# Optimization experiments

Hardware: AMD Instinct MI355X
Metric: run time of the kernel (lower is better)

Reference implementation:

```python
import jax, jax.numpy as jnp
import numpy as np

VAR = (0.1, 0.2)          # encode variances (SSD convention used in MutualGuide)
F_ALPHA, F_GAMMA = 0.25, 1.0   # FocalLoss(alpha=0.25, gamma=1.0)
L_ALPHA, L_GAMMA, L_BETA = 0.5, 1.5, 0.11  # BalancedL1Loss

def point_form(p):
    # [P,4] cxcywh -> xyxy
    return jnp.concatenate([p[:, :2] - p[:, 2:] / 2, p[:, :2] + p[:, 2:] / 2], axis=1)

def jaccard(a, b):
    # a: [T,4] xyxy truths, b: [P,4] xyxy priors -> IoU [T,P]
    lt = jnp.maximum(a[:, None, :2], b[None, :, :2])
    rb = jnp.minimum(a[:, None, 2:], b[None, :, 2:])
    wh = jnp.clip(rb - lt, 0.0)
    inter = wh[..., 0] * wh[..., 1]
    area_a = ((a[:, 2] - a[:, 0]) * (a[:, 3] - a[:, 1]))[:, None]
    area_b = ((b[:, 2] - b[:, 0]) * (b[:, 3] - b[:, 1]))[None, :]
    return inter / (area_a + area_b - inter)

def match_one(truths, labels, priors_pt):
    # truths [T,4], labels [T] int, priors_pt [P,4]
    T = truths.shape[0]
    ov = jaccard(truths, priors_pt)                 # [T,P]
    best_truth_ov = ov.max(axis=0)                  # [P]
    best_truth_idx = ov.argmax(axis=0)              # [P]
    best_prior_idx = ov.argmax(axis=1)              # [T]
    # force each gt's best prior to be positive (index_fill_ with 2)
    best_truth_ov = best_truth_ov.at[best_prior_idx].set(2.0)
    best_truth_idx = best_truth_idx.at[best_prior_idx].set(jnp.arange(T))
    matches = truths[best_truth_idx]                # [P,4] xyxy
    conf = labels[best_truth_idx] + 1               # [P], 0 reserved for bg
    return matches, conf, best_truth_ov

def encode(matched, priors):
    # matched xyxy [N,4], priors cxcywh [N.,4]
    g_cxcy = ((matched[..., :2] + matched[..., 2:]) / 2 - priors[..., :2]) / (VAR[0] * priors[..., 2:])
    g_wh = jnp.log((matched[..., 2:] - matched[..., :2]) / priors[..., 2:]) / VAR[1]
    return jnp.concatenate([g_cxcy, g_wh], axis=-1)

def balanced_l1(pred, target):
    b = np.exp(L_GAMMA / L_ALPHA) - 1.0
    d = jnp.abs(pred - target)
    small = L_ALPHA / b * (b * d + 1.0) * jnp.log(b * d / L_BETA + 1.0) - L_ALPHA * d
    large = L_GAMMA * d + L_GAMMA / b - L_ALPHA * L_BETA
    return jnp.where(d < L_BETA, small, large)

def sigmoid_focal(logits, t):
    p = jax.nn.sigmoid(logits)
    ce = -(t * jax.nn.log_sigmoid(logits) + (1.0 - t) * jax.nn.log_sigmoid(-logits))
    pt = t * (1.0 - p) + (1.0 - t) * p
    w = (F_ALPHA * t + (1.0 - F_ALPHA) * (1.0 - t)) * pt ** F_GAMMA
    return w * ce

def setup_inputs() -> dict:
    key = jax.random.key(0)
    kl, kc, kp1, kp2, kt1, kt2, ktl = jax.random.split(key, 7)
    B, P, C, T = 16, 16384, 80, 32
    loc_data = jax.random.normal(kl, (B, P, 4), jnp.float32) * 0.1
    conf_data = jax.random.normal(kc, (B, P, C), jnp.float32)
    p_cxcy = jax.random.uniform(kp1, (P, 2), jnp.float32, 0.05, 0.95)
    p_wh = jax.random.uniform(kp2, (P, 2), jnp.float32, 0.02, 0.3)
    priors = jnp.concatenate([p_cxcy, p_wh], axis=1)
    t_c = jax.random.uniform(kt1, (B, T, 2), jnp.float32, 0.2, 0.8)
    t_wh = jax.random.uniform(kt2, (B, T, 2), jnp.float32, 0.05, 0.3)
    boxes = jnp.concatenate([jnp.clip(t_c - t_wh / 2, 0.0, 1.0), jnp.clip(t_c + t_wh / 2, 0.0, 1.0)], axis=-1)
    labels = jax.random.randint(ktl, (B, T), 0, C).astype(jnp.float32)
    targets = jnp.concatenate([boxes, labels[..., None]], axis=-1)  # [B,T,5]
    return {"loc_data": loc_data, "conf_data": conf_data, "priors": priors, "targets": targets}

def reference(loc_data, conf_data, priors, targets):
    B, P, C = conf_data.shape
    truths = targets[..., :4]
    labels = targets[..., 4].astype(jnp.int32)
    priors_pt = point_form(priors)
    loc_t, conf_t, overlap_t = jax.vmap(match_one, in_axes=(0, 0, None))(truths, labels, priors_pt)
    # masks (non-mutual-guide path)
    pos = overlap_t >= 0.5                                  # [B,P]
    ign = (overlap_t < 0.5) & (overlap_t >= 0.4)
    neg = overlap_t < 0.4
    # localization loss over positives (mean over masked elements)
    loc_targets = encode(loc_t, priors[None, :, :])          # [B,P,4]
    l1 = balanced_l1(loc_data, loc_targets)                  # [B,P,4]
    n_pos = jnp.maximum(pos.sum(), 1)
    loss_l = (l1 * pos[..., None]).sum() / (4.0 * n_pos)
    # classification: one-hot minus background, flip ignored rows to -1
    conf_t = jnp.where(neg, 0, conf_t)
    onehot = jax.nn.one_hot(conf_t, C + 1, dtype=conf_data.dtype)[..., 1:]  # [B,P,C]
    batch_label = jnp.where(ign[..., None], -onehot, onehot)
    mask = batch_label >= 0
    t = jnp.where(mask, batch_label, 0.0)
    fl = sigmoid_focal(conf_data, t)
    loss_c = (fl * mask).sum() / jnp.maximum(mask.sum(), 1)
    return (loss_l, loss_c)
```

## Files before the change

kernel.cpp:

```cpp
#include <hip/hip_runtime.h>

#pragma clang fp contract(off)

#define B_SZ 16
#define P_SZ 16384
#define C_SZ 80
#define T_SZ 32

struct Partial { float l; float c; unsigned pos; unsigned ign; };

__device__ __forceinline__ float iou_ref(float ax0, float ay0, float ax1, float ay1, float aarea,
                                         float bx0, float by0, float bx1, float by1, float barea) {
    float lx = fmaxf(ax0, bx0), ly = fmaxf(ay0, by0);
    float rx = fminf(ax1, bx1), ry = fminf(ay1, by1);
    float w = fmaxf(rx - lx, 0.0f), h = fmaxf(ry - ly, 0.0f);
    float inter = w * h;
    float denom = (aarea + barea) - inter;
    return inter / denom;
}

__global__ __launch_bounds__(256) void match_kernel(const float* __restrict__ priors,
                                                    const float* __restrict__ targets,
                                                    unsigned long long* __restrict__ keys) {
    const int b = blockIdx.y;
    const int p0 = blockIdx.x * 1024;
    const int tid = threadIdx.x;

    __shared__ float tx0[T_SZ], ty0[T_SZ], tx1[T_SZ], ty1[T_SZ], tar[T_SZ];
    __shared__ float red_ov[4][T_SZ];
    __shared__ int   red_ix[4][T_SZ];

    if (tid < T_SZ) {
        const float* tp = targets + (b * T_SZ + tid) * 5;
        float x0 = tp[0], y0 = tp[1], x1 = tp[2], y1 = tp[3];
        tx0[tid] = x0; ty0[tid] = y0; tx1[tid] = x1; ty1[tid] = y1;
        tar[tid] = (x1 - x0) * (y1 - y0);
    }
    __syncthreads();

    float bov[T_SZ];
    int   bpi[T_SZ];
#pragma unroll
    for (int t = 0; t < T_SZ; ++t) { bov[t] = -1.0f; bpi[t] = 0x7FFFFFFF; }

#pragma unroll
    for (int i = 0; i < 4; ++i) {
        int p = p0 + tid + i * 256;
        float4 pr = reinterpret_cast<const float4*>(priors)[p];
        float px0 = pr.x - pr.z * 0.5f, py0 = pr.y - pr.w * 0.5f;
        float px1 = pr.x + pr.z * 0.5f, py1 = pr.y + pr.w * 0.5f;
        float parea = (px1 - px0) * (py1 - py0);
#pragma unroll
        for (int t = 0; t < T_SZ; ++t) {
            float iou = iou_ref(tx0[t], ty0[t], tx1[t], ty1[t], tar[t], px0, py0, px1, py1, parea);
            if (iou > bov[t]) { bov[t] = iou; bpi[t] = p; }
        }
    }

    const int lane = tid & 63, wid = tid >> 6;
#pragma unroll
    for (int t = 0; t < T_SZ; ++t) {
        float v = bov[t]; int ix = bpi[t];
#pragma unroll
        for (int off = 32; off > 0; off >>= 1) {
            float v2 = __shfl_down(v, off, 64);
            int   i2 = __shfl_down(ix, off, 64);
            if (v2 > v || (v2 == v && i2 < ix)) { v = v2; ix = i2; }
        }
        if (lane == 0) { red_ov[wid][t] = v; red_ix[wid][t] = ix; }
    }
    __syncthreads();

    if (tid < T_SZ) {
        float v = red_ov[0][tid]; int ix = red_ix[0][tid];
#pragma unroll
        for (int w = 1; w < 4; ++w) {
            float v2 = red_ov[w][tid]; int i2 = red_ix[w][tid];
            if (v2 > v || (v2 == v && i2 < ix)) { v = v2; ix = i2; }
        }
        unsigned long long key = (((unsigned long long)__float_as_uint(v)) << 32)
                               | (unsigned long long)(0xFFFFFFFFu - (unsigned)ix);
        keys[(b * 16 + blockIdx.x) * T_SZ + tid] = key;
    }
}

__device__ __forceinline__ float bl1(float pred, float target) {
    const float bC   = (float)19.085536923187668;
    const float aob  = (float)(0.5 / 19.085536923187668);
    const float cL   = (float)(1.5 / 19.085536923187668 - 0.055);
    float d = fabsf(pred - target);
    if (d < 0.11f) {
        return aob * (bC * d + 1.0f) * __logf(bC * d / 0.11f + 1.0f) - 0.5f * d;
    }
    return 1.5f * d + cL;
}

__device__ __forceinline__ float focal(float x, bool isT) {
    float u  = __expf(-fabsf(x));
    float L  = __logf(1.0f + u);
    float q  = __builtin_amdgcn_rcpf(1.0f + u);
    float p  = (x >= 0.0f) ? q : 1.0f - q;
    float xp = fmaxf(x, 0.0f);
    float xn = xp - x;
    return isT ? 0.25f * (1.0f - p) * (xn + L) : 0.75f * p * (xp + L);
}

__global__ __launch_bounds__(256) void loss_kernel(const float* __restrict__ loc_data,
                                                   const float* __restrict__ conf_data,
                                                   const float* __restrict__ priors,
                                                   const float* __restrict__ targets,
                                                   const unsigned long long* __restrict__ keys,
                                                   Partial* __restrict__ partials) {
    const int b = blockIdx.y;
    const int p0 = blockIdx.x * 128;
    const int tid = threadIdx.x;

    __shared__ float tx0[T_SZ], ty0[T_SZ], tx1[T_SZ], ty1[T_SZ], tar[T_SZ];
    __shared__ int tlab[T_SZ], bp[T_SZ];
    __shared__ unsigned char flag_s[128];
    __shared__ unsigned char tcls_s[128];
    __shared__ unsigned char code_s[2560];
    __shared__ float rf_l[4], rf_c[4];
    __shared__ int ri_p[4], ri_i[4];

    if (tid < T_SZ) {
        const float* tp = targets + (b * T_SZ + tid) * 5;
        float x0 = tp[0], y0 = tp[1], x1 = tp[2], y1 = tp[3];
        tx0[tid] = x0; ty0[tid] = y0; tx1[tid] = x1; ty1[tid] = y1;
        tar[tid] = (x1 - x0) * (y1 - y0);
        tlab[tid] = (int)tp[4];
        const unsigned long long* kb = keys + b * 16 * T_SZ + tid;
        unsigned long long k = kb[0];
#pragma unroll
        for (int w = 1; w < 16; ++w) {
            unsigned long long k2 = kb[w * T_SZ];
            if (k2 > k) k = k2;
        }
        bp[tid] = (int)(0xFFFFFFFFu - (unsigned)(k & 0xFFFFFFFFull));
    }
    __syncthreads();

    float sum_l = 0.0f, sum_c = 0.0f;
    int pos_c = 0, ign_c = 0;

    if (tid < 128) {
        int p = p0 + tid;
        float4 pr = reinterpret_cast<const float4*>(priors)[p];
        float px0 = pr.x - pr.z * 0.5f, py0 = pr.y - pr.w * 0.5f;
        float px1 = pr.x + pr.z * 0.5f, py1 = pr.y + pr.w * 0.5f;
        float parea = (px1 - px0) * (py1 - py0);

        float ov = -1.0f; int idx = 0;
#pragma unroll
        for (int t = 0; t < T_SZ; ++t) {
            float iou = iou_ref(tx0[t], ty0[t], tx1[t], ty1[t], tar[t], px0, py0, px1, py1, parea);
            if (iou > ov) { ov = iou; idx = t; }
        }
#pragma unroll
        for (int t = 0; t < T_SZ; ++t) if (bp[t] == p) { ov = 2.0f; idx = t; }

        int fl = (ov >= 0.5f) ? 1 : ((ov >= 0.4f) ? 2 : 0);
        flag_s[tid] = (unsigned char)fl;
        tcls_s[tid] = (unsigned char)tlab[idx];

        if (fl == 1) {
            pos_c = 1;
            float4 ld = reinterpret_cast<const float4*>(loc_data)[b * P_SZ + p];
            float mx0 = tx0[idx], my0 = ty0[idx], mx1 = tx1[idx], my1 = ty1[idx];
            float gx = ((mx0 + mx1) * 0.5f - pr.x) / (0.1f * pr.z);
            float gy = ((my0 + my1) * 0.5f - pr.y) / (0.1f * pr.w);
            float gw = __logf((mx1 - mx0) / pr.z) / 0.2f;
            float gh = __logf((my1 - my0) / pr.w) / 0.2f;
            sum_l = bl1(ld.x, gx) + bl1(ld.y, gy) + bl1(ld.z, gw) + bl1(ld.w, gh);
        } else if (fl == 2) {
            ign_c = 1;
        }
    }
    __syncthreads();

#pragma unroll
    for (int jj = tid; jj < 2560; jj += 256) {
        int pl = jj / 20;
        int c0 = (jj - pl * 20) * 4;
        int f = flag_s[pl];
        int tc = tcls_s[pl];
        int g = tc - c0;
        int m = (g >= 0 && g < 4) ? (g + 1) : 0;
        code_s[jj] = (unsigned char)(f | (m << 2));
    }
    __syncthreads();

    const float4* cbase = reinterpret_cast<const float4*>(conf_data + ((size_t)(b * P_SZ + p0)) * C_SZ);
    float4 v[10];
#pragma unroll
    for (int it = 0; it < 10; ++it) v[it] = cbase[tid + it * 256];
    unsigned char cd[10];
#pragma unroll
    for (int it = 0; it < 10; ++it) cd[it] = code_s[tid + it * 256];

#pragma unroll
    for (int it = 0; it < 10; ++it) {
        int code = cd[it];
        int f = code & 3;
        int m = code >> 2;
        float s = 0.0f;
        {
            float fk = focal(v[it].x, (f == 1) && (m == 1));
            if (!((f == 2) && (m == 1))) s += fk;
        }
        {
            float fk = focal(v[it].y, (f == 1) && (m == 2));
            if (!((f == 2) && (m == 2))) s += fk;
        }
        {
            float fk = focal(v[it].z, (f == 1) && (m == 3));
            if (!((f == 2) && (m == 3))) s += fk;
        }
        {
            float fk = focal(v[it].w, (f == 1) && (m == 4));
            if (!((f == 2) && (m == 4))) s += fk;
        }
        sum_c += s;
    }

    const int lane = tid & 63, wid = tid >> 6;
#pragma unroll
    for (int off = 32; off > 0; off >>= 1) {
        sum_l += __shfl_down(sum_l, off, 64);
        sum_c += __shfl_down(sum_c, off, 64);
        pos_c += __shfl_down(pos_c, off, 64);
        ign_c += __shfl_down(ign_c, off, 64);
    }
    if (lane == 0) { rf_l[wid] = sum_l; rf_c[wid] = sum_c; ri_p[wid] = pos_c; ri_i[wid] = ign_c; }
    __syncthreads();
    if (tid == 0) {
        Partial pt;
        pt.l = rf_l[0] + rf_l[1] + rf_l[2] + rf_l[3];
        pt.c = rf_c[0] + rf_c[1] + rf_c[2] + rf_c[3];
        pt.pos = (unsigned)(ri_p[0] + ri_p[1] + ri_p[2] + ri_p[3]);
        pt.ign = (unsigned)(ri_i[0] + ri_i[1] + ri_i[2] + ri_i[3]);
        partials[b * 128 + blockIdx.x] = pt;
    }
}

__global__ __launch_bounds__(256) void finalize_kernel(const Partial* __restrict__ partials,
                                                       float* __restrict__ out) {
    const int tid = threadIdx.x;
    __shared__ double r_l[4], r_c[4];
    __shared__ unsigned long long r_p[4], r_i[4];

    double sl = 0.0, sc = 0.0;
    unsigned long long np = 0, ni = 0;
#pragma unroll
    for (int k = 0; k < 8; ++k) {
        Partial p = partials[tid + k * 256];
        sl += (double)p.l; sc += (double)p.c;
        np += p.pos; ni += p.ign;
    }
    const int lane = tid & 63, wid = tid >> 6;
#pragma unroll
    for (int off = 32; off > 0; off >>= 1) {
        sl += __shfl_down(sl, off, 64);
        sc += __shfl_down(sc, off, 64);
        np += __shfl_down(np, off, 64);
        ni += __shfl_down(ni, off, 64);
    }
    if (lane == 0) { r_l[wid] = sl; r_c[wid] = sc; r_p[wid] = np; r_i[wid] = ni; }
    __syncthreads();
    if (tid == 0) {
        double tl = r_l[0] + r_l[1] + r_l[2] + r_l[3];
        double tc = r_c[0] + r_c[1] + r_c[2] + r_c[3];
        unsigned long long tp = r_p[0] + r_p[1] + r_p[2] + r_p[3];
        long long ti = (long long)(r_i[0] + r_i[1] + r_i[2] + r_i[3]);
        double npos = (tp < 1ull) ? 1.0 : (double)tp;
        long long msum = (long long)B_SZ * P_SZ * C_SZ - ti;
        if (msum < 1) msum = 1;
        out[0] = (float)(tl / (4.0 * npos));
        out[1] = (float)(tc / (double)msum);
    }
}

extern "C" void kernel_launch(void* const* d_in, const int* in_sizes, int n_in,
                              void* d_out, int out_size, void* d_ws, size_t ws_size,
                              hipStream_t stream) {
    const float* loc     = (const float*)d_in[0];
    const float* conf    = (const float*)d_in[1];
    const float* priors  = (const float*)d_in[2];
    const float* targets = (const float*)d_in[3];

    unsigned long long* keys = (unsigned long long*)d_ws;
    Partial* partials = (Partial*)((char*)d_ws + 65536);

    match_kernel<<<dim3(16, 16), 256, 0, stream>>>(priors, targets, keys);
    loss_kernel<<<dim3(128, 16), 256, 0, stream>>>(loc, conf, priors, targets, keys, partials);
    finalize_kernel<<<1, 256, 0, stream>>>(partials, (float*)d_out);
}
```

Before: 66.14 us.

## Split loss kernel into per-prior flags kernel and streaming focal conf kernel

The fused loss kernel, in which only half the threads did the per-prior matching before the conf sweep, is split in two. A flags kernel with all 256 threads active computes match codes into a global buffer plus the localization partials. A separate conf kernel then streams conf_data using those codes. The match kernel also uses twice as many smaller chunks for more parallelism. This adds a kernel launch and a round trip of the codes through global memory, in exchange for full thread utilisation during matching.

```diff
diff --git a/kernel.cpp b/kernel.cpp
--- a/kernel.cpp
+++ b/kernel.cpp
@@ -6,8 +6,9 @@
 #define P_SZ 16384
 #define C_SZ 80
 #define T_SZ 32
-
-struct Partial { float l; float c; unsigned pos; unsigned ign; };
+#define NCHUNK 32
+
+struct PartialL { float l; float pad; unsigned pos; unsigned ign; };
 
 __device__ __forceinline__ float iou_ref(float ax0, float ay0, float ax1, float ay1, float aarea,
                                          float bx0, float by0, float bx1, float by1, float barea) {
@@ -23,7 +24,7 @@
                                                     const float* __restrict__ targets,
                                                     unsigned long long* __restrict__ keys) {
     const int b = blockIdx.y;
-    const int p0 = blockIdx.x * 1024;
+    const int p0 = blockIdx.x * 512;
     const int tid = threadIdx.x;
 
     __shared__ float tx0[T_SZ], ty0[T_SZ], tx1[T_SZ], ty1[T_SZ], tar[T_SZ];
@@ -44,7 +45,7 @@
     for (int t = 0; t < T_SZ; ++t) { bov[t] = -1.0f; bpi[t] = 0x7FFFFFFF; }
 
 #pragma unroll
-    for (int i = 0; i < 4; ++i) {
+    for (int i = 0; i < 2; ++i) {
         int p = p0 + tid + i * 256;
         float4 pr = reinterpret_cast<const float4*>(priors)[p];
         float px0 = pr.x - pr.z * 0.5f, py0 = pr.y - pr.w * 0.5f;
@@ -80,7 +81,7 @@
         }
         unsigned long long key = (((unsigned long long)__float_as_uint(v)) << 32)
                                | (unsigned long long)(0xFFFFFFFFu - (unsigned)ix);
-        keys[(b * 16 + blockIdx.x) * T_SZ + tid] = key;
+        keys[(b * NCHUNK + blockIdx.x) * T_SZ + tid] = key;
     }
 }
 
@@ -105,23 +106,21 @@
     return isT ? 0.25f * (1.0f - p) * (xn + L) : 0.75f * p * (xp + L);
 }
 
-__global__ __launch_bounds__(256) void loss_kernel(const float* __restrict__ loc_data,
-                                                   const float* __restrict__ conf_data,
-                                                   const float* __restrict__ priors,
-                                                   const float* __restrict__ targets,
-                                                   const unsigned long long* __restrict__ keys,
-                                                   Partial* __restrict__ partials) {
+__global__ __launch_bounds__(256) void flags_kernel(const float* __restrict__ loc_data,
+                                                    const float* __restrict__ priors,
+                                                    const float* __restrict__ targets,
+                                                    const unsigned long long* __restrict__ keys,
+                                                    unsigned short* __restrict__ codes,
+                                                    PartialL* __restrict__ pl_out) {
     const int b = blockIdx.y;
-    const int p0 = blockIdx.x * 128;
+    const int p0 = blockIdx.x * 256;
     const int tid = threadIdx.x;
+    const int p = p0 + tid;
 
     __shared__ float tx0[T_SZ], ty0[T_SZ], tx1[T_SZ], ty1[T_SZ], tar[T_SZ];
     __shared__ int tlab[T_SZ], bp[T_SZ];
-    __shared__ unsigned char flag_s[128];
-    __shared__ unsigned char tcls_s[128];
-    __shared__ unsigned char code_s[2560];
-    __shared__ float rf_l[4], rf_c[4];
-    __shared__ int ri_p[4], ri_i[4];
+    __shared__ float rf[4];
+    __shared__ int rp[4], ri[4];
 
     if (tid < T_SZ) {
         const float* tp = targets + (b * T_SZ + tid) * 5;
@@ -129,10 +128,10 @@
         tx0[tid] = x0; ty0[tid] = y0; tx1[tid] = x1; ty1[tid] = y1;
         tar[tid] = (x1 - x0) * (y1 - y0);
         tlab[tid] = (int)tp[4];
-        const unsigned long long* kb = keys + b * 16 * T_SZ + tid;
+        const unsigned long long* kb = keys + b * (NCHUNK * T_SZ) + tid;
         unsigned long long k = kb[0];
 #pragma unroll
-        for (int w = 1; w < 16; ++w) {
+        for (int w = 1; w < NCHUNK; ++w) {
             unsigned long long k2 = kb[w * T_SZ];
             if (k2 > k) k = k2;
         }
@@ -140,110 +139,116 @@
     }
     __syncthreads();
 
-    float sum_l = 0.0f, sum_c = 0.0f;
+    float4 pr = reinterpret_cast<const float4*>(priors)[p];
+    float px0 = pr.x - pr.z * 0.5f, py0 = pr.y - pr.w * 0.5f;
+    float px1 = pr.x + pr.z * 0.5f, py1 = pr.y + pr.w * 0.5f;
+    float parea = (px1 - px0) * (py1 - py0);
+
+    float ov = -1.0f; int idx = 0;
+#pragma unroll
+    for (int t = 0; t < T_SZ; ++t) {
+        float iou = iou_ref(tx0[t], ty0[t], tx1[t], ty1[t], tar[t], px0, py0, px1, py1, parea);
+        if (iou > ov) { ov = iou; idx = t; }
+    }
+#pragma unroll
+    for (int t = 0; t < T_SZ; ++t) if (bp[t] == p) { ov = 2.0f; idx = t; }
+
+    int fl = (ov >= 0.5f) ? 1 : ((ov >= 0.4f) ? 2 : 0);
+    int tc = tlab[idx];
+    codes[b * P_SZ + p] = (unsigned short)((tc << 2) | fl);
+
+    float sum_l = 0.0f;
     int pos_c = 0, ign_c = 0;
-
-    if (tid < 128) {
-        int p = p0 + tid;
-        float4 pr = reinterpret_cast<const float4*>(priors)[p];
-        float px0 = pr.x - pr.z * 0.5f, py0 = pr.y - pr.w * 0.5f;
-        float px1 = pr.x + pr.z * 0.5f, py1 = pr.y + pr.w * 0.5f;
-        float parea = (px1 - px0) * (py1 - py0);
-
-        float ov = -1.0f; int idx = 0;
-#pragma unroll
-        for (int t = 0; t < T_SZ; ++t) {
-            float iou = iou_ref(tx0[t], ty0[t], tx1[t], ty1[t], tar[t], px0, py0, px1, py1, parea);
-            if (iou > ov) { ov = iou; idx = t; }
-        }
-#pragma unroll
-        for (int t = 0; t < T_SZ; ++t) if (bp[t] == p) { ov = 2.0f; idx = t; }
-
-        int fl = (ov >= 0.5f) ? 1 : ((ov >= 0.4f) ? 2 : 0);
-        flag_s[tid] = (unsigned char)fl;
-        tcls_s[tid] = (unsigned char)tlab[idx];
-
-        if (fl == 1) {
-            pos_c = 1;
-            float4 ld = reinterpret_cast<const float4*>(loc_data)[b * P_SZ + p];
-            float mx0 = tx0[idx], my0 = ty0[idx], mx1 = tx1[idx], my1 = ty1[idx];
-            float gx = ((mx0 + mx1) * 0.5f - pr.x) / (0.1f * pr.z);
-            float gy = ((my0 + my1) * 0.5f - pr.y) / (0.1f * pr.w);
-            float gw = __logf((mx1 - mx0) / pr.z) / 0.2f;
-            float gh = __logf((my1 - my0) / pr.w) / 0.2f;
-            sum_l = bl1(ld.x, gx) + bl1(ld.y, gy) + bl1(ld.z, gw) + bl1(ld.w, gh);
-        } else if (fl == 2) {
-            ign_c = 1;
-        }
-    }
-    __syncthreads();
-
-#pragma unroll
-    for (int jj = tid; jj < 2560; jj += 256) {
-        int pl = jj / 20;
-        int c0 = (jj - pl * 20) * 4;
-        int f = flag_s[pl];
-        int tc = tcls_s[pl];
-        int g = tc - c0;
-        int m = (g >= 0 && g < 4) ? (g + 1) : 0;
-        code_s[jj] = (unsigned char)(f | (m << 2));
-    }
-    __syncthreads();
+    if (fl == 1) {
+        pos_c = 1;
+        float4 ld = reinterpret_cast<const float4*>(loc_data)[b * P_SZ + p];
+        float mx0 = tx0[idx], my0 = ty0[idx], mx1 = tx1[idx], my1 = ty1[idx];
+        float gx = ((mx0 + mx1) * 0.5f - pr.x) / (0.1f * pr.z);
+        float gy = ((my0 + my1) * 0.5f - pr.y) / (0.1f * pr.w);
+        float gw = __logf((mx1 - mx0) / pr.z) / 0.2f;
+        float gh = __logf((my1 - my0) / pr.w) / 0.2f;
+        sum_l = bl1(ld.x, gx) + bl1(ld.y, gy) + bl1(ld.z, gw) + bl1(ld.w, gh);
+    } else if (fl == 2) {
+        ign_c = 1;
+    }
+
+    const int lane = tid & 63, wid = tid >> 6;
+#pragma unroll
+    for (int off = 32; off > 0; off >>= 1) {
+        sum_l += __shfl_down(sum_l, off, 64);
+        pos_c += __shfl_down(pos_c, off, 64);
+        ign_c += __shfl_down(ign_c, off, 64);
+    }
+    if (lane == 0) { rf[wid] = sum_l; rp[wid] = pos_c; ri[wid] = ign_c; }
+    __syncthreads();
+    if (tid == 0) {
+        PartialL o;
+        o.l = rf[0] + rf[1] + rf[2] + rf[3];
+        o.pad = 0.0f;
+        o.pos = (unsigned)(rp[0] + rp[1] + rp[2] + rp[3]);
+        o.ign = (unsigned)(ri[0] + ri[1] + ri[2] + ri[3]);
+        pl_out[b * 64 + blockIdx.x] = o;
+    }
+}
+
+__global__ __launch_bounds__(256) void conf_kernel(const float* __restrict__ conf_data,
+                                                   const unsigned short* __restrict__ codes,
+                                                   float* __restrict__ pc_out) {
+    const int b = blockIdx.y;
+    const int p0 = blockIdx.x * 128;
+    const int tid = threadIdx.x;
 
     const float4* cbase = reinterpret_cast<const float4*>(conf_data + ((size_t)(b * P_SZ + p0)) * C_SZ);
+    const unsigned short* cdb = codes + b * P_SZ + p0;
+
     float4 v[10];
-#pragma unroll
-    for (int it = 0; it < 10; ++it) v[it] = cbase[tid + it * 256];
-    unsigned char cd[10];
-#pragma unroll
-    for (int it = 0; it < 10; ++it) cd[it] = code_s[tid + it * 256];
-
+    unsigned short cd[10];
 #pragma unroll
     for (int it = 0; it < 10; ++it) {
-        int code = cd[it];
-        int f = code & 3;
-        int m = code >> 2;
+        int j = tid + it * 256;
+        v[it] = cbase[j];
+        cd[it] = cdb[j / 20];
+    }
+
+    float sum_c = 0.0f;
+#pragma unroll
+    for (int it = 0; it < 10; ++it) {
+        int j = tid + it * 256;
+        int pl = j / 20;
+        int c0 = (j - pl * 20) * 4;
+        int f = cd[it] & 3;
+        int g = (cd[it] >> 2) - c0;
         float s = 0.0f;
         {
-            float fk = focal(v[it].x, (f == 1) && (m == 1));
-            if (!((f == 2) && (m == 1))) s += fk;
+            float fk = focal(v[it].x, (f == 1) && (g == 0));
+            if (!((f == 2) && (g == 0))) s += fk;
         }
         {
-            float fk = focal(v[it].y, (f == 1) && (m == 2));
-            if (!((f == 2) && (m == 2))) s += fk;
+            float fk = focal(v[it].y, (f == 1) && (g == 1));
+            if (!((f == 2) && (g == 1))) s += fk;
         }
         {
-            float fk = focal(v[it].z, (f == 1) && (m == 3));
-            if (!((f == 2) && (m == 3))) s += fk;
+            float fk = focal(v[it].z, (f == 1) && (g == 2));
+            if (!((f == 2) && (g == 2))) s += fk;
         }
         {
-            float fk = focal(v[it].w, (f == 1) && (m == 4));
-            if (!((f == 2) && (m == 4))) s += fk;
+            float fk = focal(v[it].w, (f == 1) && (g == 3));
+            if (!((f == 2) && (g == 3))) s += fk;
         }
         sum_c += s;
     }
 
+    __shared__ float rf[4];
     const int lane = tid & 63, wid = tid >> 6;
 #pragma unroll
-    for (int off = 32; off > 0; off >>= 1) {
-        sum_l += __shfl_down(sum_l, off, 64);
-        sum_c += __shfl_down(sum_c, off, 64);
-        pos_c += __shfl_down(pos_c, off, 64);
-        ign_c += __shfl_down(ign_c, off, 64);
-    }
-    if (lane == 0) { rf_l[wid] = sum_l; rf_c[wid] = sum_c; ri_p[wid] = pos_c; ri_i[wid] = ign_c; }
-    __syncthreads();
-    if (tid == 0) {
-        Partial pt;
-        pt.l = rf_l[0] + rf_l[1] + rf_l[2] + rf_l[3];
-        pt.c = rf_c[0] + rf_c[1] + rf_c[2] + rf_c[3];
-        pt.pos = (unsigned)(ri_p[0] + ri_p[1] + ri_p[2] + ri_p[3]);
-        pt.ign = (unsigned)(ri_i[0] + ri_i[1] + ri_i[2] + ri_i[3]);
-        partials[b * 128 + blockIdx.x] = pt;
-    }
-}
-
-__global__ __launch_bounds__(256) void finalize_kernel(const Partial* __restrict__ partials,
+    for (int off = 32; off > 0; off >>= 1) sum_c += __shfl_down(sum_c, off, 64);
+    if (lane == 0) rf[wid] = sum_c;
+    __syncthreads();
+    if (tid == 0) pc_out[b * 128 + blockIdx.x] = rf[0] + rf[1] + rf[2] + rf[3];
+}
+
+__global__ __launch_bounds__(256) void finalize_kernel(const PartialL* __restrict__ pl,
+                                                       const float* __restrict__ pc,
                                                        float* __restrict__ out) {
     const int tid = threadIdx.x;
     __shared__ double r_l[4], r_c[4];
@@ -252,11 +257,13 @@
     double sl = 0.0, sc = 0.0;
     unsigned long long np = 0, ni = 0;
 #pragma unroll
-    for (int k = 0; k < 8; ++k) {
-        Partial p = partials[tid + k * 256];
-        sl += (double)p.l; sc += (double)p.c;
-        np += p.pos; ni += p.ign;
-    }
+    for (int k = 0; k < 4; ++k) {
+        PartialL p = pl[tid + k * 256];
+        sl += (double)p.l; np += p.pos; ni += p.ign;
+    }
+#pragma unroll
+    for (int k = 0; k < 8; ++k) sc += (double)pc[tid + k * 256];
+
     const int lane = tid & 63, wid = tid >> 6;
 #pragma unroll
     for (int off = 32; off > 0; off >>= 1) {
@@ -288,10 +295,14 @@
     const float* priors  = (const float*)d_in[2];
     const float* targets = (const float*)d_in[3];
 
-    unsigned long long* keys = (unsigned long long*)d_ws;
-    Partial* partials = (Partial*)((char*)d_ws + 65536);
-
-    match_kernel<<<dim3(16, 16), 256, 0, stream>>>(priors, targets, keys);
-    loss_kernel<<<dim3(128, 16), 256, 0, stream>>>(loc, conf, priors, targets, keys, partials);
-    finalize_kernel<<<1, 256, 0, stream>>>(partials, (float*)d_out);
-}
+    char* ws = (char*)d_ws;
+    unsigned long long* keys = (unsigned long long*)ws;
+    unsigned short*    codes = (unsigned short*)(ws + 131072);
+    PartialL*          plp   = (PartialL*)(ws + 655360);
+    float*             pcp   = (float*)(ws + 671744);
+
+    match_kernel<<<dim3(NCHUNK, 16), 256, 0, stream>>>(priors, targets, keys);
+    flags_kernel<<<dim3(64, 16), 256, 0, stream>>>(loc, priors, targets, keys, codes, plp);
+    conf_kernel<<<dim3(128, 16), 256, 0, stream>>>(conf, codes, pcp);
+    finalize_kernel<<<1, 256, 0, stream>>>(plp, pcp, (float*)d_out);
+}
```

Measured after the change: 65.48 us. No clear change (-1.0%).
